# Kernel optimization log

Measured on AMD Instinct MI355X. Metric: run time of the kernel, lower is better.

The kernel has to match this reference:

```python
import jax, jax.numpy as jnp
import numpy as np

D_MODEL = 1024
N_HEADS = 16
HEAD_DIM = 64
BATCH = 4
SEQ = 2048


def setup_inputs() -> dict:
    key = jax.random.key(0)
    ks = jax.random.split(key, 5)
    scale = 1.0 / np.sqrt(D_MODEL)
    return {
        "x": jax.random.normal(ks[0], (BATCH, SEQ, D_MODEL), dtype=jnp.float32),
        "Wq": jax.random.normal(ks[1], (D_MODEL, N_HEADS * HEAD_DIM), dtype=jnp.float32) * scale,
        "Wk": jax.random.normal(ks[2], (D_MODEL, N_HEADS * HEAD_DIM), dtype=jnp.float32) * scale,
        "Wv": jax.random.normal(ks[3], (D_MODEL, N_HEADS * HEAD_DIM), dtype=jnp.float32) * scale,
        "Wo": jax.random.normal(ks[4], (N_HEADS * HEAD_DIM, D_MODEL), dtype=jnp.float32) * scale,
        "bo": jnp.zeros((D_MODEL,), dtype=jnp.float32),
    }


def reference(x, Wq, Wk, Wv, Wo, bo):
    B, S, _ = x.shape
    H, Dh = N_HEADS, HEAD_DIM
    # projections -> [B, H, S, Dh]
    q = (x @ Wq).reshape(B, S, H, Dh).transpose(0, 2, 1, 3)
    k = (x @ Wk).reshape(B, S, H, Dh).transpose(0, 2, 1, 3)
    v = (x @ Wv).reshape(B, S, H, Dh).transpose(0, 2, 1, 3)
    score = jnp.einsum("bhsd,bhtd->bhst", q, k) / jnp.sqrt(jnp.float32(Dh))
    causal = jnp.triu(jnp.ones((S, S), dtype=bool), k=1)
    score = jnp.where(causal, -jnp.inf, score)
    attn_probs = jax.nn.softmax(score, axis=-1)
    # dropout is identity in eval mode
    attn = jnp.einsum("bhst,bhtd->bhsd", attn_probs, v)
    out = attn.transpose(0, 2, 1, 3).reshape(B, S, H * Dh)
    out = out @ Wo + bo
    return (out, attn_probs)
```

## Files before the change

kernel.cpp:

```cpp
#include <hip/hip_runtime.h>
#include <hip/hip_bf16.h>

typedef __attribute__((ext_vector_type(8))) short bf16x8;
typedef __attribute__((ext_vector_type(4))) float f32x4;
typedef unsigned short ushort_t;
typedef unsigned int uint_t;

#define AS1 __attribute__((address_space(1)))
#define AS3 __attribute__((address_space(3)))

__constant__ int P4tab[16] = {0, 5, 10, 15, 1, 4, 11, 14, 2, 7, 8, 13, 3, 6, 9, 12};

__device__ __forceinline__ void gload_lds16(const void* g, void* l) {
    __builtin_amdgcn_global_load_lds((const AS1 void*)g, (AS3 void*)l, 16, 0, 0);
}

__device__ __forceinline__ ushort_t f2b(float f) {
    unsigned u = __builtin_bit_cast(unsigned, f);
    unsigned r = (u + 0x7FFFu + ((u >> 16) & 1u)) >> 16;
    return (ushort_t)r;
}

__global__ __launch_bounds__(256) void convert_x_kernel(const float* __restrict__ in,
                                                        ushort_t* __restrict__ out, int n4) {
    int i = blockIdx.x * blockDim.x + threadIdx.x;
    if (i < n4) {
        float4 f = ((const float4*)in)[i];
        ushort4 u;
        u.x = f2b(f.x); u.y = f2b(f.y); u.z = f2b(f.z); u.w = f2b(f.w);
        ((ushort4*)out)[i] = u;
    }
}

__global__ __launch_bounds__(256) void transpose_w_kernel(const float* __restrict__ W,
                                                          ushort_t* __restrict__ WT) {
    __shared__ float t[32][33];
    int n0 = blockIdx.x * 32, k0 = blockIdx.y * 32;
    int tx = threadIdx.x, ty = threadIdx.y;
    for (int i = 0; i < 4; ++i)
        t[ty + i * 8][tx] = W[(size_t)(k0 + ty + i * 8) * 1024 + n0 + tx];
    __syncthreads();
    for (int i = 0; i < 4; ++i)
        WT[(size_t)(n0 + ty + i * 8) * 1024 + k0 + tx] = f2b(t[tx][ty + i * 8]);
}

template <int N, int OUT_BF16>
__global__ __launch_bounds__(256) void gemm_kernel(const ushort_t* __restrict__ A,
                                                   const ushort_t* __restrict__ BT,
                                                   ushort_t* __restrict__ Cb,
                                                   float* __restrict__ Cf,
                                                   const float* __restrict__ bias) {
    const int K = 1024;
    __shared__ ushort_t As[2 * 128 * 32];
    __shared__ ushort_t Bs[2 * 128 * 32];
    int tid = threadIdx.x;
    int wid = tid >> 6, lane = tid & 63;
    int g = lane >> 4, lr = lane & 15;
    int m0 = blockIdx.x * 128, n0 = blockIdx.y * 128;
    int wm = wid >> 1, wn = wid & 1;

    f32x4 acc[4][4] = {};

    int c0 = wid * 2;
    int lrow = lane >> 2;
    int lcol = ((lane & 3) ^ ((lane >> 3) & 3)) * 8;
    const ushort_t* Ag0 = A  + (size_t)(m0 + c0 * 16 + lrow) * K + lcol;
    const ushort_t* Ag1 = A  + (size_t)(m0 + c0 * 16 + 16 + lrow) * K + lcol;
    const ushort_t* Bg0 = BT + (size_t)(n0 + c0 * 16 + lrow) * K + lcol;
    const ushort_t* Bg1 = BT + (size_t)(n0 + c0 * 16 + 16 + lrow) * K + lcol;

    int swzA = ((lr >> 1) & 3) << 4;

    auto stage = [&](int bufi, int kt) {
        char* a0 = (char*)As + bufi * 8192 + c0 * 1024;
        char* b0 = (char*)Bs + bufi * 8192 + c0 * 1024;
        gload_lds16(Ag0 + kt * 32, a0);
        gload_lds16(Ag1 + kt * 32, a0 + 1024);
        gload_lds16(Bg0 + kt * 32, b0);
        gload_lds16(Bg1 + kt * 32, b0 + 1024);
    };

    stage(0, 0);
    __syncthreads();
    int buf = 0;
    for (int kt = 0; kt < K / 32; ++kt) {
        if (kt + 1 < K / 32) stage(buf ^ 1, kt + 1);
        const char* ab = (const char*)As + buf * 8192;
        const char* bb = (const char*)Bs + buf * 8192;
        bf16x8 af[4], bfr[4];
#pragma unroll
        for (int m = 0; m < 4; ++m) {
            int row = wm * 64 + m * 16 + lr;
            af[m] = *(const bf16x8*)(ab + row * 64 + ((g * 16) ^ swzA));
        }
#pragma unroll
        for (int n = 0; n < 4; ++n) {
            int row = wn * 64 + n * 16 + lr;
            bfr[n] = *(const bf16x8*)(bb + row * 64 + ((g * 16) ^ swzA));
        }
#pragma unroll
        for (int m = 0; m < 4; ++m)
#pragma unroll
            for (int n = 0; n < 4; ++n)
                acc[m][n] = __builtin_amdgcn_mfma_f32_16x16x32_bf16(af[m], bfr[n], acc[m][n], 0, 0, 0);
        __syncthreads();
        buf ^= 1;
    }

#pragma unroll
    for (int m = 0; m < 4; ++m)
#pragma unroll
        for (int n = 0; n < 4; ++n) {
            int row0 = m0 + wm * 64 + m * 16 + g * 4;
            int col  = n0 + wn * 64 + n * 16 + lr;
#pragma unroll
            for (int r = 0; r < 4; ++r) {
                float v = acc[m][n][r];
                if (OUT_BF16)
                    Cb[(size_t)(row0 + r) * N + col] = f2b(v);
                else
                    Cf[(size_t)(row0 + r) * N + col] = v + bias[col];
            }
        }
}

__global__ __launch_bounds__(256) void vt_kernel(const ushort_t* __restrict__ Cqkv,
                                                 ushort_t* __restrict__ Vt) {
    int b = blockIdx.z, h = blockIdx.y, st = blockIdx.x;
    __shared__ ushort_t t[64][72];
    const ushort_t* src = Cqkv + (size_t)b * 2048 * 3072 + 2048 + (size_t)h * 64;
    int tid = threadIdx.x;
#pragma unroll
    for (int i = 0; i < 2; ++i) {
        int c = tid + i * 256;
        int sl = c >> 3, dc = (c & 7) * 8;
        *(bf16x8*)&t[sl][dc] = *(const bf16x8*)(src + (size_t)(st * 64 + sl) * 3072 + dc);
    }
    __syncthreads();
#pragma unroll
    for (int i = 0; i < 2; ++i) {
        int c = tid + i * 256;
        int d = c >> 3, sc = (c & 7) * 8;
        bf16x8 v;
#pragma unroll
        for (int j = 0; j < 8; ++j) v[j] = (short)t[sc + j][d];
        *(bf16x8*)(Vt + ((size_t)(b * 16 + h) * 64 + d) * 2048 + st * 64 + sc) = v;
    }
}

__global__ __launch_bounds__(256, 4) void attn_kernel(const ushort_t* __restrict__ Cqkv,
                                                      const ushort_t* __restrict__ Vtg,
                                                      float* __restrict__ Pout,
                                                      ushort_t* __restrict__ Oout) {
    const int S = 2048, DQ = 3072;
    const float C1 = 0.18033688f;
    const float C2 = 5.77078016f;

    int z = (int)blockIdx.x;
    int c = z & 255, j = z >> 8;
    int p = P4tab[(c & 3) * 4 + j];
    int h = (c >> 2) & 15, b = c >> 6;
    int qtA = p, qtB = 31 - p;

    int tid = threadIdx.x, wid = tid >> 6, lane = tid & 63;
    int g = lane >> 4, lr = lane & 15;

    __shared__ ushort_t KV[4][4096];
    __shared__ ushort_t Pl[4096];
    char* PlB = (char*)Pl + wid * 2048;

    const ushort_t* Qb = Cqkv + (size_t)b * S * DQ + (size_t)h * 64;
    const ushort_t* Kb = Cqkv + (size_t)b * S * DQ + 1024 + (size_t)h * 64;
    const ushort_t* Vb = Vtg + (size_t)((b * 16 + h) * 64) * 2048;
    float* PbaseA = Pout + (((size_t)(b * 16 + h)) * S + qtA * 64) * S;
    float* PbaseB = Pout + (((size_t)(b * 16 + h)) * S + qtB * 64) * S;

    int srow = lane >> 3;
    int scol = ((lane & 7) ^ srow) * 8;

    auto stageK = [&](int ri, int tt) {
        char* dst = (char*)&KV[ri][0] + wid * 1024;
        gload_lds16(Kb + (size_t)(tt * 64 + wid * 8 + srow) * DQ + scol, dst);
        gload_lds16(Kb + (size_t)(tt * 64 + 32 + wid * 8 + srow) * DQ + scol, dst + 4096);
    };
    auto stageV = [&](int ri, int tt) {
        char* dst = (char*)&KV[2 + ri][0] + wid * 1024;
        gload_lds16(Vb + (size_t)(wid * 8 + srow) * 2048 + tt * 64 + scol, dst);
        gload_lds16(Vb + (size_t)(32 + wid * 8 + srow) * 2048 + tt * 64 + scol, dst + 4096);
    };

    bf16x8 qfA[2], qfB[2];
    {
        const ushort_t* qa = Qb + (size_t)(qtA * 64 + wid * 16 + lr) * DQ + g * 8;
        qfA[0] = *(const bf16x8*)qa;
        qfA[1] = *(const bf16x8*)(qa + 32);
        const ushort_t* qb2 = Qb + (size_t)(qtB * 64 + wid * 16 + lr) * DQ + g * 8;
        qfB[0] = *(const bf16x8*)qb2;
        qfB[1] = *(const bf16x8*)(qb2 + 32);
    }
    int qloc = wid * 16 + lr;

    float psA = 0.f, psB = 0.f;
    stageK(0, 0);
    stageK(1, 1);
    asm volatile("s_waitcnt vmcnt(8)" ::: "memory");
    __builtin_amdgcn_s_barrier();
    __builtin_amdgcn_sched_barrier(0);
    for (int tt = 0; tt <= qtB; ++tt) {
        int nt = tt + 2;
        stageK(nt & 3, nt <= qtB ? nt : qtB);
        const char* ksb = (const char*)&KV[tt & 3][0];
        __builtin_amdgcn_s_setprio(1);
#pragma unroll
        for (int nb = 0; nb < 4; ++nb) {
            int row = nb * 16 + lr;
            int x = (row & 7) << 4;
            bf16x8 k0 = *(const bf16x8*)(ksb + row * 128 + ((g * 16) ^ x));
            bf16x8 k1 = *(const bf16x8*)(ksb + row * 128 + ((64 + g * 16) ^ x));
            f32x4 sB = {};
            sB = __builtin_amdgcn_mfma_f32_16x16x32_bf16(k0, qfB[0], sB, 0, 0, 0);
            sB = __builtin_amdgcn_mfma_f32_16x16x32_bf16(k1, qfB[1], sB, 0, 0, 0);
            if (tt == qtB) {
#pragma unroll
                for (int r = 0; r < 4; ++r)
                    if (nb * 16 + g * 4 + r <= qloc) psB += exp2f(fmaf(sB[r], C1, -C2));
            } else {
#pragma unroll
                for (int r = 0; r < 4; ++r) psB += exp2f(fmaf(sB[r], C1, -C2));
            }
            if (tt <= qtA) {
                f32x4 sA = {};
                sA = __builtin_amdgcn_mfma_f32_16x16x32_bf16(k0, qfA[0], sA, 0, 0, 0);
                sA = __builtin_amdgcn_mfma_f32_16x16x32_bf16(k1, qfA[1], sA, 0, 0, 0);
                if (tt == qtA) {
#pragma unroll
                    for (int r = 0; r < 4; ++r)
                        if (nb * 16 + g * 4 + r <= qloc) psA += exp2f(fmaf(sA[r], C1, -C2));
                } else {
#pragma unroll
                    for (int r = 0; r < 4; ++r) psA += exp2f(fmaf(sA[r], C1, -C2));
                }
            }
        }
        __builtin_amdgcn_s_setprio(0);
        asm volatile("s_waitcnt vmcnt(8)" ::: "memory");
        __builtin_amdgcn_s_barrier();
        __builtin_amdgcn_sched_barrier(0);
    }
    asm volatile("s_waitcnt vmcnt(0)" ::: "memory");
    psA += __shfl_xor(psA, 16); psA += __shfl_xor(psA, 32);
    psB += __shfl_xor(psB, 16); psB += __shfl_xor(psB, 32);
    float lnA = __log2f(psA) + C2;
    float lnB = __log2f(psB) + C2;

    f32x4 OA[4] = {}, OB[4] = {};
    stageK(0, 0);
    stageV(0, 0);
    __syncthreads();
    int buf = 0;
    for (int tt = 0; tt <= qtB; ++tt) {
        if (tt < qtB) { stageK(buf ^ 1, tt + 1); stageV(buf ^ 1, tt + 1); }
        const char* ksb = (const char*)&KV[buf][0];
        const char* vsb = (const char*)&KV[2 + buf][0];

        {
            f32x4 pv[4];
            __builtin_amdgcn_s_setprio(1);
#pragma unroll
            for (int nb = 0; nb < 4; ++nb) {
                int row = nb * 16 + lr;
                int x = (row & 7) << 4;
                f32x4 s = {};
                s = __builtin_amdgcn_mfma_f32_16x16x32_bf16(*(const bf16x8*)(ksb + row * 128 + ((g * 16) ^ x)), qfB[0], s, 0, 0, 0);
                s = __builtin_amdgcn_mfma_f32_16x16x32_bf16(*(const bf16x8*)(ksb + row * 128 + ((64 + g * 16) ^ x)), qfB[1], s, 0, 0, 0);
#pragma unroll
                for (int r = 0; r < 4; ++r) {
                    float v = exp2f(fmaf(s[r], C1, -lnB));
                    if (tt == qtB && (nb * 16 + g * 4 + r > qloc)) v = 0.f;
                    pv[nb][r] = v;
                }
            }
            __builtin_amdgcn_s_setprio(0);
#pragma unroll
            for (int nb = 0; nb < 4; ++nb)
                *(f32x4*)(PbaseB + (size_t)qloc * S + tt * 64 + nb * 16 + g * 4) = pv[nb];
#pragma unroll
            for (int nb = 0; nb < 4; ++nb) {
                uint_t w0, w1;
                asm("v_cvt_pk_bf16_f32 %0, %1, %2" : "=v"(w0) : "v"(pv[nb][0]), "v"(pv[nb][1]));
                asm("v_cvt_pk_bf16_f32 %0, %1, %2" : "=v"(w1) : "v"(pv[nb][2]), "v"(pv[nb][3]));
                uint2 w; w.x = w0; w.y = w1;
                *(uint2*)(PlB + ((lr * 128 + nb * 32 + g * 8) ^ ((lr & 7) << 4))) = w;
            }
            __builtin_amdgcn_wave_barrier();
            __builtin_amdgcn_s_setprio(1);
#pragma unroll
            for (int kc = 0; kc < 2; ++kc) {
                bf16x8 pf = *(const bf16x8*)(PlB + ((lr * 128 + kc * 64 + g * 16) ^ ((lr & 7) << 4)));
#pragma unroll
                for (int nb = 0; nb < 4; ++nb) {
                    int vrow = nb * 16 + lr;
                    bf16x8 vf = *(const bf16x8*)(vsb + vrow * 128 + ((kc * 64 + g * 16) ^ ((vrow & 7) << 4)));
                    OB[nb] = __builtin_amdgcn_mfma_f32_16x16x32_bf16(pf, vf, OB[nb], 0, 0, 0);
                }
            }
            __builtin_amdgcn_s_setprio(0);
            __builtin_amdgcn_wave_barrier();
        }

        if (tt <= qtA) {
            f32x4 pv[4];
            __builtin_amdgcn_s_setprio(1);
#pragma unroll
            for (int nb = 0; nb < 4; ++nb) {
                int row = nb * 16 + lr;
                int x = (row & 7) << 4;
                f32x4 s = {};
                s = __builtin_amdgcn_mfma_f32_16x16x32_bf16(*(const bf16x8*)(ksb + row * 128 + ((g * 16) ^ x)), qfA[0], s, 0, 0, 0);
                s = __builtin_amdgcn_mfma_f32_16x16x32_bf16(*(const bf16x8*)(ksb + row * 128 + ((64 + g * 16) ^ x)), qfA[1], s, 0, 0, 0);
#pragma unroll
                for (int r = 0; r < 4; ++r) {
                    float v = exp2f(fmaf(s[r], C1, -lnA));
                    if (tt == qtA && (nb * 16 + g * 4 + r > qloc)) v = 0.f;
                    pv[nb][r] = v;
                }
            }
            __builtin_amdgcn_s_setprio(0);
#pragma unroll
            for (int nb = 0; nb < 4; ++nb)
                *(f32x4*)(PbaseA + (size_t)qloc * S + tt * 64 + nb * 16 + g * 4) = pv[nb];
#pragma unroll
            for (int nb = 0; nb < 4; ++nb) {
                uint_t w0, w1;
                asm("v_cvt_pk_bf16_f32 %0, %1, %2" : "=v"(w0) : "v"(pv[nb][0]), "v"(pv[nb][1]));
                asm("v_cvt_pk_bf16_f32 %0, %1, %2" : "=v"(w1) : "v"(pv[nb][2]), "v"(pv[nb][3]));
                uint2 w; w.x = w0; w.y = w1;
                *(uint2*)(PlB + ((lr * 128 + nb * 32 + g * 8) ^ ((lr & 7) << 4))) = w;
            }
            __builtin_amdgcn_wave_barrier();
            __builtin_amdgcn_s_setprio(1);
#pragma unroll
            for (int kc = 0; kc < 2; ++kc) {
                bf16x8 pf = *(const bf16x8*)(PlB + ((lr * 128 + kc * 64 + g * 16) ^ ((lr & 7) << 4)));
#pragma unroll
                for (int nb = 0; nb < 4; ++nb) {
                    int vrow = nb * 16 + lr;
                    bf16x8 vf = *(const bf16x8*)(vsb + vrow * 128 + ((kc * 64 + g * 16) ^ ((vrow & 7) << 4)));
                    OA[nb] = __builtin_amdgcn_mfma_f32_16x16x32_bf16(pf, vf, OA[nb], 0, 0, 0);
                }
            }
            __builtin_amdgcn_s_setprio(0);
            __builtin_amdgcn_wave_barrier();
            asm volatile("s_waitcnt vmcnt(8)" ::: "memory");
        } else {
            asm volatile("s_waitcnt vmcnt(4)" ::: "memory");
        }
        __builtin_amdgcn_s_barrier();
        __builtin_amdgcn_sched_barrier(0);
        buf ^= 1;
    }

    {
        int vsr = tid >> 2, vsc = (tid & 3) * 16;
        float4 zf = {0.f, 0.f, 0.f, 0.f};
        for (int tt = qtA + 1; tt < 32; ++tt) {
            float* dst = PbaseA + (size_t)vsr * S + tt * 64 + vsc;
#pragma unroll
            for (int jj = 0; jj < 4; ++jj) ((float4*)dst)[jj] = zf;
        }
        for (int tt = qtB + 1; tt < 32; ++tt) {
            float* dst = PbaseB + (size_t)vsr * S + tt * 64 + vsc;
#pragma unroll
            for (int jj = 0; jj < 4; ++jj) ((float4*)dst)[jj] = zf;
        }
    }

#pragma unroll
    for (int nb = 0; nb < 4; ++nb)
#pragma unroll
        for (int r = 0; r < 4; ++r) {
            int qA = qtA * 64 + wid * 16 + g * 4 + r;
            int qB = qtB * 64 + wid * 16 + g * 4 + r;
            Oout[((size_t)b * S + qA) * 1024 + h * 64 + nb * 16 + lr] = f2b(OA[nb][r]);
            Oout[((size_t)b * S + qB) * 1024 + h * 64 + nb * 16 + lr] = f2b(OB[nb][r]);
        }
}

extern "C" void kernel_launch(void* const* d_in, const int* in_sizes, int n_in,
                              void* d_out, int out_size, void* d_ws, size_t ws_size,
                              hipStream_t stream) {
    const float* x  = (const float*)d_in[0];
    const float* Wq = (const float*)d_in[1];
    const float* Wk = (const float*)d_in[2];
    const float* Wv = (const float*)d_in[3];
    const float* Wo = (const float*)d_in[4];
    const float* bo = (const float*)d_in[5];

    float* out  = (float*)d_out;
    float* Pout = out + (size_t)8388608;

    char* ws = (char*)d_ws;
    ushort_t* xb    = (ushort_t*)(ws);
    ushort_t* wqkv  = (ushort_t*)(ws + (16u << 20));
    ushort_t* wob   = (ushort_t*)(ws + (22u << 20));
    ushort_t* Cqkv  = (ushort_t*)(ws + (24u << 20));
    ushort_t* Vtw   = (ushort_t*)(ws + (72u << 20));
    ushort_t* attnb = (ushort_t*)(ws + (104u << 20));

    convert_x_kernel<<<8192, 256, 0, stream>>>(x, xb, 2097152);
    transpose_w_kernel<<<dim3(32, 32), dim3(32, 8), 0, stream>>>(Wq, wqkv);
    transpose_w_kernel<<<dim3(32, 32), dim3(32, 8), 0, stream>>>(Wk, wqkv + 1024 * 1024);
    transpose_w_kernel<<<dim3(32, 32), dim3(32, 8), 0, stream>>>(Wv, wqkv + 2 * 1024 * 1024);
    transpose_w_kernel<<<dim3(32, 32), dim3(32, 8), 0, stream>>>(Wo, wob);

    gemm_kernel<3072, 1><<<dim3(64, 24), 256, 0, stream>>>(xb, wqkv, Cqkv, nullptr, nullptr);

    vt_kernel<<<dim3(32, 16, 4), 256, 0, stream>>>(Cqkv, Vtw);

    attn_kernel<<<1024, 256, 0, stream>>>(Cqkv, Vtw, Pout, attnb);

    gemm_kernel<1024, 0><<<dim3(64, 8), 256, 0, stream>>>(attnb, wob, nullptr, out, bo);
}
```

Baseline: 482.7 us.

## Triple-buffer GEMM with swizzled block order and pair K tiles in softmax pass

The projection GEMM moves from a double-buffered LDS pipeline with __syncthreads to a three-stage ring, prefetching two k-tiles ahead with explicit vmcnt waits and raw barriers. It also remaps block indices so consecutive workgroups are spread in groups of eight, likely to improve L2 or XCD locality. In the attention row-sum pass, K tiles are now staged two at a time with one barrier per pair instead of per tile, but each step waits on vmcnt(0), which can expose load latency. LDS use in the GEMM goes up by half.

```diff
diff --git a/kernel.cpp b/kernel.cpp
--- a/kernel.cpp
+++ b/kernel.cpp
@@ -51,12 +51,17 @@
                                                    float* __restrict__ Cf,
                                                    const float* __restrict__ bias) {
     const int K = 1024;
-    __shared__ ushort_t As[2 * 128 * 32];
-    __shared__ ushort_t Bs[2 * 128 * 32];
+    __shared__ ushort_t As[3 * 128 * 32];
+    __shared__ ushort_t Bs[3 * 128 * 32];
     int tid = threadIdx.x;
     int wid = tid >> 6, lane = tid & 63;
     int g = lane >> 4, lr = lane & 15;
-    int m0 = blockIdx.x * 128, n0 = blockIdx.y * 128;
+
+    int zz = (int)blockIdx.x + 64 * (int)blockIdx.y;
+    int nwg = 64 * (int)gridDim.y;
+    int zs = (zz & 7) * (nwg >> 3) + (zz >> 3);
+    int m0 = (zs % 64) * 128, n0 = (zs / 64) * 128;
+
     int wm = wid >> 1, wn = wid & 1;
 
     f32x4 acc[4][4] = {};
@@ -71,9 +76,9 @@
 
     int swzA = ((lr >> 1) & 3) << 4;
 
-    auto stage = [&](int bufi, int kt) {
-        char* a0 = (char*)As + bufi * 8192 + c0 * 1024;
-        char* b0 = (char*)Bs + bufi * 8192 + c0 * 1024;
+    auto stage = [&](int si, int kt) {
+        char* a0 = (char*)As + si * 8192 + c0 * 1024;
+        char* b0 = (char*)Bs + si * 8192 + c0 * 1024;
         gload_lds16(Ag0 + kt * 32, a0);
         gload_lds16(Ag1 + kt * 32, a0 + 1024);
         gload_lds16(Bg0 + kt * 32, b0);
@@ -81,12 +86,15 @@
     };
 
     stage(0, 0);
-    __syncthreads();
-    int buf = 0;
-    for (int kt = 0; kt < K / 32; ++kt) {
-        if (kt + 1 < K / 32) stage(buf ^ 1, kt + 1);
-        const char* ab = (const char*)As + buf * 8192;
-        const char* bb = (const char*)Bs + buf * 8192;
+    stage(1, 1);
+    asm volatile("s_waitcnt vmcnt(4)" ::: "memory");
+    __builtin_amdgcn_s_barrier();
+    __builtin_amdgcn_sched_barrier(0);
+    for (int kt = 0; kt < 32; ++kt) {
+        int nt = kt + 2;
+        stage(nt % 3, nt < 32 ? nt : 31);
+        const char* ab = (const char*)As + (kt % 3) * 8192;
+        const char* bb = (const char*)Bs + (kt % 3) * 8192;
         bf16x8 af[4], bfr[4];
 #pragma unroll
         for (int m = 0; m < 4; ++m) {
@@ -103,8 +111,9 @@
 #pragma unroll
             for (int n = 0; n < 4; ++n)
                 acc[m][n] = __builtin_amdgcn_mfma_f32_16x16x32_bf16(af[m], bfr[n], acc[m][n], 0, 0, 0);
-        __syncthreads();
-        buf ^= 1;
+        asm volatile("s_waitcnt vmcnt(4)" ::: "memory");
+        __builtin_amdgcn_s_barrier();
+        __builtin_amdgcn_sched_barrier(0);
     }
 
 #pragma unroll
@@ -188,6 +197,13 @@
         gload_lds16(Vb + (size_t)(wid * 8 + srow) * 2048 + tt * 64 + scol, dst);
         gload_lds16(Vb + (size_t)(32 + wid * 8 + srow) * 2048 + tt * 64 + scol, dst + 4096);
     };
+    auto stageK2 = [&](int ss, int t0, int t1) {
+        char* dst = (char*)&KV[ss * 2][0] + wid * 1024;
+        gload_lds16(Kb + (size_t)(t0 * 64 + wid * 8 + srow) * DQ + scol, dst);
+        gload_lds16(Kb + (size_t)(t0 * 64 + 32 + wid * 8 + srow) * DQ + scol, dst + 4096);
+        gload_lds16(Kb + (size_t)(t1 * 64 + wid * 8 + srow) * DQ + scol, dst + 8192);
+        gload_lds16(Kb + (size_t)(t1 * 64 + 32 + wid * 8 + srow) * DQ + scol, dst + 12288);
+    };
 
     bf16x8 qfA[2], qfB[2];
     {
@@ -201,16 +217,8 @@
     int qloc = wid * 16 + lr;
 
     float psA = 0.f, psB = 0.f;
-    stageK(0, 0);
-    stageK(1, 1);
-    asm volatile("s_waitcnt vmcnt(8)" ::: "memory");
-    __builtin_amdgcn_s_barrier();
-    __builtin_amdgcn_sched_barrier(0);
-    for (int tt = 0; tt <= qtB; ++tt) {
-        int nt = tt + 2;
-        stageK(nt & 3, nt <= qtB ? nt : qtB);
-        const char* ksb = (const char*)&KV[tt & 3][0];
-        __builtin_amdgcn_s_setprio(1);
+
+    auto p1_tile = [&](const char* ksb, int tt) {
 #pragma unroll
         for (int nb = 0; nb < 4; ++nb) {
             int row = nb * 16 + lr;
@@ -242,12 +250,27 @@
                 }
             }
         }
+    };
+
+    int nR = (qtB + 2) >> 1;
+    stageK2(0, 0, 1);
+    asm volatile("s_waitcnt vmcnt(0)" ::: "memory");
+    __builtin_amdgcn_s_barrier();
+    __builtin_amdgcn_sched_barrier(0);
+    for (int ri = 0; ri < nR; ++ri) {
+        int t0n = 2 * ri + 2, t1n = 2 * ri + 3;
+        if (t0n > qtB) t0n = qtB;
+        if (t1n > qtB) t1n = qtB;
+        stageK2((ri + 1) & 1, t0n, t1n);
+        const char* ksb = (const char*)&KV[(ri & 1) * 2][0];
+        __builtin_amdgcn_s_setprio(1);
+        p1_tile(ksb, 2 * ri);
+        if (2 * ri + 1 <= qtB) p1_tile(ksb + 8192, 2 * ri + 1);
         __builtin_amdgcn_s_setprio(0);
-        asm volatile("s_waitcnt vmcnt(8)" ::: "memory");
+        asm volatile("s_waitcnt vmcnt(0)" ::: "memory");
         __builtin_amdgcn_s_barrier();
         __builtin_amdgcn_sched_barrier(0);
     }
-    asm volatile("s_waitcnt vmcnt(0)" ::: "memory");
     psA += __shfl_xor(psA, 16); psA += __shfl_xor(psA, 32);
     psB += __shfl_xor(psB, 16); psB += __shfl_xor(psB, 32);
     float lnA = __log2f(psA) + C2;
```

New measurement: 488.0 us. About the same (+1.1%).
